# Optimization experiments

Measured on AMD Instinct MI355X. Metric: run time of the kernel, lower is better.

Reference implementation:

```python
import jax, jax.numpy as jnp
import numpy as np

N_NODES, N_EDGES, C_IN = 50000, 320000, 512
DIMS = [C_IN, 2048, 1024, 512, 256, 128]


def setup_inputs() -> dict:
    key = jax.random.key(0)
    ks = jax.random.split(key, 2 + 2 * 5)
    inp = {
        "x": jax.random.normal(ks[0], (N_NODES, C_IN), jnp.float32),
        "edge_index": jax.random.randint(ks[1], (2, N_EDGES), 0, N_NODES, dtype=jnp.int64),
    }
    for i in range(5):
        fan_in = DIMS[i]
        inp[f"W{i+1}"] = jax.random.normal(ks[2 + 2 * i], (DIMS[i], DIMS[i + 1]), jnp.float32) / np.float32(np.sqrt(fan_in))
        inp[f"b{i+1}"] = jnp.zeros((DIMS[i + 1],), jnp.float32)
    return inp


def _gcn_layer(h, W, b, src, dst, dinv, n_nodes):
    # PyG GCNConv: h' = D^{-1/2} (A + I) D^{-1/2} (h W) + b, deg includes self-loop
    h = h @ W                                  # [N, out]
    norm = (dinv[src] * dinv[dst])[:, None]    # per-edge normalization
    agg = jax.ops.segment_sum(h[src] * norm, dst, num_segments=n_nodes)
    agg = agg + h * (dinv * dinv)[:, None]     # self-loop contribution
    return agg + b


def reference(x, edge_index, W1, b1, W2, b2, W3, b3, W4, b4, W5, b5):
    n = x.shape[0]
    src, dst = edge_index[0], edge_index[1]
    # in-degree (at dst) + 1 for self-loop, as in PyG gcn_norm
    deg = jax.ops.segment_sum(jnp.ones(src.shape[0], x.dtype), dst, num_segments=n) + 1.0
    dinv = jax.lax.rsqrt(deg)
    # dropout is identity in eval mode (training=False)
    h = jax.nn.relu(_gcn_layer(x, W1, b1, src, dst, dinv, n))
    h = jax.nn.relu(_gcn_layer(h, W2, b2, src, dst, dinv, n))
    h = jax.nn.relu(_gcn_layer(h, W3, b3, src, dst, dinv, n))
    h = jax.nn.relu(_gcn_layer(h, W4, b4, src, dst, dinv, n))
    return _gcn_layer(h, W5, b5, src, dst, dinv, n)
```

## Files before the change

kernel.cpp:

```cpp
#include <hip/hip_runtime.h>
#include <hip/hip_bf16.h>
#include <stdint.h>

#define N_NODES 50000
#define N_EDGES 320000
#define MP 50048

typedef __hip_bfloat16 bf16_t;
typedef __attribute__((ext_vector_type(8))) short short8;
typedef __attribute__((ext_vector_type(4))) float floatx4;

__global__ void detect_kernel(const int* __restrict__ ei, int* __restrict__ flag) {
    if (blockIdx.x == 0 && threadIdx.x == 0) {
        int any_nonzero = 0;
        for (int i = 0; i < 128; ++i)
            if (ei[2 * i + 1] != 0) any_nonzero = 1;
        *flag = any_nonzero ? 0 : 1;
    }
}

__device__ __forceinline__ int load_edge(const int* ei, int row, int e, int is64) {
    long pos = (long)row * N_EDGES + e;
    return is64 ? ei[2 * pos] : ei[pos];
}

__global__ void count_kernel(const int* __restrict__ ei, const int* __restrict__ flag,
                             int* __restrict__ counts) {
    int e = blockIdx.x * 256 + threadIdx.x;
    if (e < N_EDGES) {
        int d = load_edge(ei, 1, e, *flag);
        atomicAdd(&counts[d], 1);
    }
}

__global__ __launch_bounds__(1024)
void scan_kernel(const int* __restrict__ counts, int* __restrict__ rowptr,
                 int* __restrict__ cursor, float* __restrict__ dinv) {
    __shared__ int wsum[16];
    __shared__ int base_s;
    int tid  = threadIdx.x;
    int lane = tid & 63;
    int wv   = tid >> 6;
    if (tid == 0) base_s = 0;
    __syncthreads();
    for (int start = 0; start < N_NODES; start += 1024) {
        int i = start + tid;
        int v = (i < N_NODES) ? counts[i] : 0;
        int s = v;
#pragma unroll
        for (int off = 1; off < 64; off <<= 1) {
            int t = __shfl_up(s, off, 64);
            if (lane >= off) s += t;
        }
        if (lane == 63) wsum[wv] = s;
        __syncthreads();
        if (wv == 0 && lane < 16) {
            int t = wsum[lane];
#pragma unroll
            for (int off = 1; off < 16; off <<= 1) {
                int u = __shfl_up(t, off, 64);
                if (lane >= off) t += u;
            }
            wsum[lane] = t;
        }
        __syncthreads();
        int wbase = (wv == 0) ? 0 : wsum[wv - 1];
        int incl  = s + wbase;
        int base  = base_s;
        if (i < N_NODES) {
            int excl = base + incl - v;
            rowptr[i] = excl;
            cursor[i] = excl;
            dinv[i] = rsqrtf((float)v + 1.0f);
        }
        __syncthreads();
        if (tid == 1023) base_s = base + incl;
        __syncthreads();
    }
    if (tid == 0) rowptr[N_NODES] = N_EDGES;
}

__global__ void fill_kernel(const int* __restrict__ ei, const int* __restrict__ flag,
                            int* __restrict__ cursor, int* __restrict__ esrc) {
    int e = blockIdx.x * 256 + threadIdx.x;
    if (e < N_EDGES) {
        int is64 = *flag;
        int s = load_edge(ei, 0, e, is64);
        int d = load_edge(ei, 1, e, is64);
        int p = atomicAdd(&cursor[d], 1);
        esrc[p] = s;
    }
}

__global__ void cast_x_kernel(const float* __restrict__ x, bf16_t* __restrict__ xb) {
    long idx = ((long)blockIdx.x * 256 + threadIdx.x) * 4;
    if (idx >= (long)MP * 512) return;
    union { bf16_t h[4]; uint2 u; } o;
    long row = idx >> 9;
    if (row < N_NODES) {
        float4 v = *(const float4*)(x + idx);
        o.h[0] = __float2bfloat16(v.x);
        o.h[1] = __float2bfloat16(v.y);
        o.h[2] = __float2bfloat16(v.z);
        o.h[3] = __float2bfloat16(v.w);
    } else {
        o.u = make_uint2(0u, 0u);
    }
    *(uint2*)(xb + idx) = o.u;
}

__global__ void cast_w_kernel(const float* __restrict__ W, bf16_t* __restrict__ Wt,
                              int K, int Nn) {
    int idx = blockIdx.x * 256 + threadIdx.x;
    if (idx >= K * Nn) return;
    int n = idx % Nn;
    int k = idx / Nn;
    Wt[(size_t)n * K + k] = __float2bfloat16(W[idx]);
}

#define BM 128
#define BN 128
#define BK 64

__device__ __forceinline__ void stage16(const bf16_t* g, bf16_t* l) {
    __builtin_amdgcn_global_load_lds(
        (const __attribute__((address_space(1))) void*)g,
        (__attribute__((address_space(3))) void*)l, 16, 0, 0);
}

__global__ __launch_bounds__(256)
void gemm_bf16(const bf16_t* __restrict__ A, const bf16_t* __restrict__ Bt,
               bf16_t* __restrict__ C, int K, int Nn,
               const float* __restrict__ bias, int relu, int nx, int ny) {
    int id   = blockIdx.x;
    int xcd  = id & 7;
    int slot = id >> 3;
    int y    = (slot / nx) * 8 + xcd;
    int xt   = slot % nx;
    if (y >= ny) return;

    __shared__ __align__(16) bf16_t ldsA[BM * BK];
    __shared__ __align__(16) bf16_t ldsB[BN * BK];

    int tid  = threadIdx.x;
    int lane = tid & 63;
    int wave = tid >> 6;
    int m15  = lane & 15;
    int quad = lane >> 4;
    int wm = (wave & 1) * 64;
    int wn = (wave >> 1) * 64;
    long bm0 = (long)y * BM;
    long bn0 = (long)xt * BN;

    floatx4 acc[4][4] = {};

    int rb   = tid >> 3;
    int cole = ((tid & 7) ^ (rb & 7)) * 8;
    const bf16_t* pa = A  + (bm0 + rb) * (long)K + cole;
    const bf16_t* pb = Bt + (bn0 + rb) * (long)K + cole;
    bf16_t* la = ldsA + tid * 8;
    bf16_t* lb = ldsB + tid * 8;
    const long step32 = 32 * (long)K;

    int fx   = lane & 7;
    int blk0 = ((0 + quad) ^ fx) * 8;
    int blk1 = ((4 + quad) ^ fx) * 8;
    int rowA = (wm + m15) * BK;
    int rowB = (wn + m15) * BK;

    for (int k0 = 0; k0 < K; k0 += BK) {
#pragma unroll
        for (int it = 0; it < 4; ++it) {
            stage16(pa + it * step32, la + it * 2048);
            stage16(pb + it * step32, lb + it * 2048);
        }
        pa += BK;
        pb += BK;
        __syncthreads();
#pragma unroll
        for (int kk = 0; kk < 2; ++kk) {
            int blk = kk ? blk1 : blk0;
            short8 af[4], bfr[4];
#pragma unroll
            for (int i = 0; i < 4; ++i)
                af[i] = *(const short8*)(&ldsA[rowA + i * (16 * BK) + blk]);
#pragma unroll
            for (int j = 0; j < 4; ++j)
                bfr[j] = *(const short8*)(&ldsB[rowB + j * (16 * BK) + blk]);
#pragma unroll
            for (int i = 0; i < 4; ++i)
#pragma unroll
                for (int j = 0; j < 4; ++j)
                    acc[i][j] = __builtin_amdgcn_mfma_f32_16x16x32_bf16(af[i], bfr[j], acc[i][j], 0, 0, 0);
        }
        __syncthreads();
    }

#pragma unroll
    for (int i = 0; i < 4; ++i) {
#pragma unroll
        for (int j = 0; j < 4; ++j) {
            long row0 = bm0 + wm + i * 16 + quad * 4;
            long col  = bn0 + wn + j * 16 + m15;
            float bv = bias ? bias[col] : 0.f;
#pragma unroll
            for (int r = 0; r < 4; ++r) {
                float v = acc[i][j][r] + bv;
                if (relu) v = fmaxf(v, 0.f);
                C[(row0 + r) * (long)Nn + col] = __float2bfloat16(v);
            }
        }
    }
}

__device__ __forceinline__ void unpack8(uint4 v, float* f) {
    uint32_t u[4] = {v.x, v.y, v.z, v.w};
#pragma unroll
    for (int i = 0; i < 4; ++i) {
        f[2 * i]     = __uint_as_float(u[i] << 16);
        f[2 * i + 1] = __uint_as_float(u[i] & 0xffff0000u);
    }
}

__global__ __launch_bounds__(256)
void agg_kernel(const bf16_t* __restrict__ hW, const int* __restrict__ rowptr,
                const int* __restrict__ esrc, const float* __restrict__ dinv,
                const float* __restrict__ bias, bf16_t* __restrict__ outb,
                float* __restrict__ outf, int Nn, int chunks, int relu, int rows) {
    int wave = threadIdx.x >> 6;
    int lane = threadIdx.x & 63;
    long unit = (long)blockIdx.x * 4 + wave;
    if (unit >= (long)rows * chunks) return;
    int n     = (int)(unit / chunks);
    int chunk = (int)(unit % chunks);
    int c0 = chunk * 512 + lane * 8;
    if (c0 >= Nn) return;

    if (n >= N_NODES) {
        if (outb) *(uint4*)(outb + (size_t)n * Nn + c0) = make_uint4(0, 0, 0, 0);
        return;
    }

    float dn = dinv[n];
    int r0 = rowptr[n], r1 = rowptr[n + 1];
    float acc[8] = {};

    uint4 v_cur; float w_cur = 0.f;
    if (r0 < r1) {
        int s = esrc[r0];
        w_cur = dinv[s] * dn;
        v_cur = *(const uint4*)(hW + (size_t)s * Nn + c0);
    }
    for (int e = r0; e < r1; ++e) {
        uint4 v = v_cur; float w = w_cur;
        if (e + 1 < r1) {
            int s2 = esrc[e + 1];
            w_cur = dinv[s2] * dn;
            v_cur = *(const uint4*)(hW + (size_t)s2 * Nn + c0);
        }
        float fv[8]; unpack8(v, fv);
#pragma unroll
        for (int j = 0; j < 8; ++j) acc[j] += fv[j] * w;
    }

    {
        uint4 v = *(const uint4*)(hW + (size_t)n * Nn + c0);
        float fv[8]; unpack8(v, fv);
        float w = dn * dn;
#pragma unroll
        for (int j = 0; j < 8; ++j) acc[j] += fv[j] * w;
    }
    if (bias) {
#pragma unroll
        for (int j = 0; j < 8; ++j) acc[j] += bias[c0 + j];
    }
    if (relu) {
#pragma unroll
        for (int j = 0; j < 8; ++j) acc[j] = fmaxf(acc[j], 0.f);
    }
    if (outf) {
        *(float4*)(outf + (size_t)n * Nn + c0)     = make_float4(acc[0], acc[1], acc[2], acc[3]);
        *(float4*)(outf + (size_t)n * Nn + c0 + 4) = make_float4(acc[4], acc[5], acc[6], acc[7]);
    } else {
        union { bf16_t h[8]; uint4 u; } o;
#pragma unroll
        for (int j = 0; j < 8; ++j) o.h[j] = __float2bfloat16(acc[j]);
        *(uint4*)(outb + (size_t)n * Nn + c0) = o.u;
    }
}

extern "C" void kernel_launch(void* const* d_in, const int* in_sizes, int n_in,
                              void* d_out, int out_size, void* d_ws, size_t ws_size,
                              hipStream_t stream) {
    (void)in_sizes; (void)n_in; (void)out_size; (void)ws_size;
    const float* x  = (const float*)d_in[0];
    const int*   ei = (const int*)d_in[1];
    const float* W[5] = {(const float*)d_in[2], (const float*)d_in[4], (const float*)d_in[6],
                         (const float*)d_in[8], (const float*)d_in[10]};
    const float* B[5] = {(const float*)d_in[3], (const float*)d_in[5], (const float*)d_in[7],
                         (const float*)d_in[9], (const float*)d_in[11]};
    static const int dims[6] = {512, 2048, 1024, 512, 256, 128};

    const size_t SZ_A = (size_t)MP * 512 * 2;
    const size_t SZ_B = (size_t)MP * 512 * 2;
    const size_t SZ_C = (size_t)MP * 2048 * 2;
    char* base = (char*)d_ws;
    bf16_t* regA = (bf16_t*)base;
    bf16_t* regB = (bf16_t*)(base + SZ_A);
    bf16_t* regC = (bf16_t*)(base + SZ_A + SZ_B);
    char* p = base + SZ_A + SZ_B + SZ_C;
    auto take = [&](size_t bytes) { char* r = p; p += (bytes + 255) & ~(size_t)255; return r; };
    bf16_t* wt[5];
    for (int i = 0; i < 5; ++i) wt[i] = (bf16_t*)take((size_t)dims[i] * dims[i + 1] * 2);
    int*   counts = (int*)take((size_t)N_NODES * 4);
    int*   rowptr = (int*)take((size_t)(N_NODES + 1) * 4);
    int*   cursor = (int*)take((size_t)N_NODES * 4);
    int*   esrc   = (int*)take((size_t)N_EDGES * 4);
    float* dinv   = (float*)take((size_t)N_NODES * 4);
    int*   eflag  = (int*)take(256);

    detect_kernel<<<1, 64, 0, stream>>>(ei, eflag);
    hipMemsetAsync(counts, 0, (size_t)N_NODES * 4, stream);
    count_kernel<<<(N_EDGES + 255) / 256, 256, 0, stream>>>(ei, eflag, counts);
    scan_kernel<<<1, 1024, 0, stream>>>(counts, rowptr, cursor, dinv);
    fill_kernel<<<(N_EDGES + 255) / 256, 256, 0, stream>>>(ei, eflag, cursor, esrc);

    bf16_t* xb = regA;
    cast_x_kernel<<<(int)(((long)MP * 512 / 4 + 255) / 256), 256, 0, stream>>>(x, xb);
    for (int i = 0; i < 5; ++i) {
        int kn = dims[i] * dims[i + 1];
        cast_w_kernel<<<(kn + 255) / 256, 256, 0, stream>>>(W[i], wt[i], dims[i], dims[i + 1]);
    }

    auto launch_gemm = [&](const bf16_t* a, const bf16_t* bt, bf16_t* c,
                           int K, int Nn, const float* bias, int relu) {
        int nx = Nn / BN;
        int ny = MP / BM;
        int blocks = nx * (((ny + 7) / 8) * 8);
        gemm_bf16<<<blocks, 256, 0, stream>>>(a, bt, c, K, Nn, bias, relu, nx, ny);
    };

    auto launch_agg = [&](const bf16_t* hw, const float* bias, bf16_t* outb,
                          float* outf, int Nn, int relu, int rows) {
        int chunks = (Nn + 511) / 512;
        long units = (long)rows * chunks;
        int blocks = (int)((units + 3) / 4);
        agg_kernel<<<blocks, 256, 0, stream>>>(hw, rowptr, esrc, dinv, bias,
                                               outb, outf, Nn, chunks, relu, rows);
    };

    bf16_t* g1 = regB;
    bf16_t* h1 = regC;
    launch_agg(xb, nullptr, g1, nullptr, 512, 0, MP);
    launch_gemm(g1, wt[0], h1, 512, 2048, B[0], 1);

    bf16_t* hwbuf[4] = {regA, regA, regA, regA};
    bf16_t* hbuf[3]  = {regC, regB, regB};
    const bf16_t* hin = h1;
    for (int l = 1; l < 5; ++l) {
        int K = dims[l], Nn = dims[l + 1];
        bf16_t* hw = hwbuf[l - 1];
        launch_gemm(hin, wt[l], hw, K, Nn, nullptr, 0);
        if (l < 4) {
            bf16_t* hn = hbuf[l - 1];
            launch_agg(hw, B[l], hn, nullptr, Nn, 1, MP);
            hin = hn;
        } else {
            launch_agg(hw, B[l], nullptr, (float*)d_out, Nn, 0, N_NODES);
        }
    }
}
```

Baseline: 1.183 ms.

## Precompute per-edge weights and unroll aggregation loop by four

Edge normalization weights dinv[s]*dinv[d] are now computed once in the CSR fill kernel and stored next to esrc, and self-loop weights are precomputed in the scan. This removes the dependent dinv gather from every aggregation layer. The aggregation loop is unrolled to issue four independent row gathers at a time, replacing the one-deep software prefetch, to raise memory-level parallelism. The detect kernel now uses a wave ballot instead of a serial loop. The cost is an extra per-edge weight array and more registers in the aggregation kernel.

Result: faster. 1.112 ms (-6.0%).

```diff
diff --git a/kernel.cpp b/kernel.cpp
--- a/kernel.cpp
+++ b/kernel.cpp
@@ -11,12 +11,10 @@
 typedef __attribute__((ext_vector_type(4))) float floatx4;
 
 __global__ void detect_kernel(const int* __restrict__ ei, int* __restrict__ flag) {
-    if (blockIdx.x == 0 && threadIdx.x == 0) {
-        int any_nonzero = 0;
-        for (int i = 0; i < 128; ++i)
-            if (ei[2 * i + 1] != 0) any_nonzero = 1;
-        *flag = any_nonzero ? 0 : 1;
-    }
+    int tid = threadIdx.x;
+    int v = ei[2 * tid + 1];
+    unsigned long long b = __ballot(v != 0);
+    if (tid == 0) *flag = (b == 0ull) ? 1 : 0;
 }
 
 __device__ __forceinline__ int load_edge(const int* ei, int row, int e, int is64) {
@@ -35,7 +33,8 @@
 
 __global__ __launch_bounds__(1024)
 void scan_kernel(const int* __restrict__ counts, int* __restrict__ rowptr,
-                 int* __restrict__ cursor, float* __restrict__ dinv) {
+                 int* __restrict__ cursor, float* __restrict__ dinv,
+                 float* __restrict__ selfw) {
     __shared__ int wsum[16];
     __shared__ int base_s;
     int tid  = threadIdx.x;
@@ -71,7 +70,9 @@
             int excl = base + incl - v;
             rowptr[i] = excl;
             cursor[i] = excl;
-            dinv[i] = rsqrtf((float)v + 1.0f);
+            float di = rsqrtf((float)v + 1.0f);
+            dinv[i] = di;
+            selfw[i] = di * di;
         }
         __syncthreads();
         if (tid == 1023) base_s = base + incl;
@@ -81,7 +82,8 @@
 }
 
 __global__ void fill_kernel(const int* __restrict__ ei, const int* __restrict__ flag,
-                            int* __restrict__ cursor, int* __restrict__ esrc) {
+                            int* __restrict__ cursor, const float* __restrict__ dinv,
+                            int* __restrict__ esrc, float* __restrict__ ewt) {
     int e = blockIdx.x * 256 + threadIdx.x;
     if (e < N_EDGES) {
         int is64 = *flag;
@@ -89,6 +91,7 @@
         int d = load_edge(ei, 1, e, is64);
         int p = atomicAdd(&cursor[d], 1);
         esrc[p] = s;
+        ewt[p]  = dinv[s] * dinv[d];
     }
 }
 
@@ -224,7 +227,8 @@
 
 __global__ __launch_bounds__(256)
 void agg_kernel(const bf16_t* __restrict__ hW, const int* __restrict__ rowptr,
-                const int* __restrict__ esrc, const float* __restrict__ dinv,
+                const int* __restrict__ esrc, const float* __restrict__ ewt,
+                const float* __restrict__ selfw,
                 const float* __restrict__ bias, bf16_t* __restrict__ outb,
                 float* __restrict__ outf, int Nn, int chunks, int relu, int rows) {
     int wave = threadIdx.x >> 6;
@@ -241,23 +245,27 @@
         return;
     }
 
-    float dn = dinv[n];
     int r0 = rowptr[n], r1 = rowptr[n + 1];
     float acc[8] = {};
 
-    uint4 v_cur; float w_cur = 0.f;
-    if (r0 < r1) {
-        int s = esrc[r0];
-        w_cur = dinv[s] * dn;
-        v_cur = *(const uint4*)(hW + (size_t)s * Nn + c0);
-    }
-    for (int e = r0; e < r1; ++e) {
-        uint4 v = v_cur; float w = w_cur;
-        if (e + 1 < r1) {
-            int s2 = esrc[e + 1];
-            w_cur = dinv[s2] * dn;
-            v_cur = *(const uint4*)(hW + (size_t)s2 * Nn + c0);
-        }
+    int e = r0;
+    for (; e + 4 <= r1; e += 4) {
+        int s0 = esrc[e], s1 = esrc[e + 1], s2 = esrc[e + 2], s3 = esrc[e + 3];
+        float w0 = ewt[e], w1 = ewt[e + 1], w2 = ewt[e + 2], w3 = ewt[e + 3];
+        uint4 v0 = *(const uint4*)(hW + (size_t)s0 * Nn + c0);
+        uint4 v1 = *(const uint4*)(hW + (size_t)s1 * Nn + c0);
+        uint4 v2 = *(const uint4*)(hW + (size_t)s2 * Nn + c0);
+        uint4 v3 = *(const uint4*)(hW + (size_t)s3 * Nn + c0);
+        float f0[8], f1[8], f2[8], f3[8];
+        unpack8(v0, f0); unpack8(v1, f1); unpack8(v2, f2); unpack8(v3, f3);
+#pragma unroll
+        for (int j = 0; j < 8; ++j)
+            acc[j] += f0[j] * w0 + f1[j] * w1 + f2[j] * w2 + f3[j] * w3;
+    }
+    for (; e < r1; ++e) {
+        int s = esrc[e];
+        float w = ewt[e];
+        uint4 v = *(const uint4*)(hW + (size_t)s * Nn + c0);
         float fv[8]; unpack8(v, fv);
 #pragma unroll
         for (int j = 0; j < 8; ++j) acc[j] += fv[j] * w;
@@ -266,7 +274,7 @@
     {
         uint4 v = *(const uint4*)(hW + (size_t)n * Nn + c0);
         float fv[8]; unpack8(v, fv);
-        float w = dn * dn;
+        float w = selfw[n];
 #pragma unroll
         for (int j = 0; j < 8; ++j) acc[j] += fv[j] * w;
     }
@@ -316,14 +324,16 @@
     int*   rowptr = (int*)take((size_t)(N_NODES + 1) * 4);
     int*   cursor = (int*)take((size_t)N_NODES * 4);
     int*   esrc   = (int*)take((size_t)N_EDGES * 4);
+    float* ewt    = (float*)take((size_t)N_EDGES * 4);
     float* dinv   = (float*)take((size_t)N_NODES * 4);
+    float* selfw  = (float*)take((size_t)N_NODES * 4);
     int*   eflag  = (int*)take(256);
 
     detect_kernel<<<1, 64, 0, stream>>>(ei, eflag);
     hipMemsetAsync(counts, 0, (size_t)N_NODES * 4, stream);
     count_kernel<<<(N_EDGES + 255) / 256, 256, 0, stream>>>(ei, eflag, counts);
-    scan_kernel<<<1, 1024, 0, stream>>>(counts, rowptr, cursor, dinv);
-    fill_kernel<<<(N_EDGES + 255) / 256, 256, 0, stream>>>(ei, eflag, cursor, esrc);
+    scan_kernel<<<1, 1024, 0, stream>>>(counts, rowptr, cursor, dinv, selfw);
+    fill_kernel<<<(N_EDGES + 255) / 256, 256, 0, stream>>>(ei, eflag, cursor, dinv, esrc, ewt);
 
     bf16_t* xb = regA;
     cast_x_kernel<<<(int)(((long)MP * 512 / 4 + 255) / 256), 256, 0, stream>>>(x, xb);
@@ -345,7 +355,7 @@
         int chunks = (Nn + 511) / 512;
         long units = (long)rows * chunks;
         int blocks = (int)((units + 3) / 4);
-        agg_kernel<<<blocks, 256, 0, stream>>>(hw, rowptr, esrc, dinv, bias,
+        agg_kernel<<<blocks, 256, 0, stream>>>(hw, rowptr, esrc, ewt, selfw, bias,
                                                outb, outf, Nn, chunks, relu, rows);
     };
 
```
